# Performance work log

Measured on AMD Instinct MI355X. Metric: run time of the kernel, lower is better.

Reference implementation:

```python
import jax, jax.numpy as jnp
import numpy as np

L, B, D = 2048, 4, 1024
H = 16
DK = D // 2            # q/k dim = 512
GLU_D = 2816
D_CONV = 4
NORMALIZER = 16.0
EPS = 1e-5


def setup_inputs() -> dict:
    key = jax.random.key(0)
    ks = jax.random.split(key, 20)
    s = 0.02
    inp = {
        "x": jax.random.normal(ks[0], (L, B, D), jnp.float32),
        "tn_w": jnp.ones((D,), jnp.float32),
        "tn_b": jnp.zeros((D,), jnp.float32),
        "conv_w": jax.random.normal(ks[1], (D, D_CONV), jnp.float32) * s,  # depthwise kernel (d, w)
        "q_w": jax.random.normal(ks[2], (D, DK), jnp.float32) * s,
        "kg_w": jax.random.normal(ks[3], (D, DK), jnp.float32) * s,
        "v_w": jax.random.normal(ks[4], (D, D), jnp.float32) * s,
        "g_w": jax.random.normal(ks[5], (D, D), jnp.float32) * s,
        "g_b": jnp.zeros((D,), jnp.float32),
        "out_w": jax.random.normal(ks[6], (D, D), jnp.float32) * s,
        "aug_balance": jax.random.normal(ks[7], (DK,), jnp.float32) * s,
        "cn_w": jnp.ones((D,), jnp.float32),
        "cn_b": jnp.zeros((D,), jnp.float32),
        "l1_w": jax.random.normal(ks[8], (D, GLU_D), jnp.float32) * s,
        "l2_w": jax.random.normal(ks[9], (D, GLU_D), jnp.float32) * s,
        "l3_w": jax.random.normal(ks[10], (GLU_D, D), jnp.float32) * s,
    }
    return inp


def _layernorm(y, w, b):
    m = jnp.mean(y, axis=-1, keepdims=True)
    v = jnp.var(y, axis=-1, keepdims=True)
    return (y - m) * jax.lax.rsqrt(v + EPS) * w + b


def _gla_scan(q, k, v, gk):
    # q,k,gk: (B,H,L,dk); v: (B,H,L,dv). Recurrent gated linear attention:
    # S_t = diag(exp(gk_t)) S_{t-1} + k_t v_t^T ; o_t = q_t S_t
    b, h, l, dk = q.shape
    dv = v.shape[-1]
    qT = jnp.moveaxis(q, 2, 0)  # (L,B,H,dk)
    kT = jnp.moveaxis(k, 2, 0)
    vT = jnp.moveaxis(v, 2, 0)
    gT = jnp.moveaxis(gk, 2, 0)

    def step(S, inp):
        q_t, k_t, v_t, g_t = inp
        S = jnp.exp(g_t)[..., None] * S + k_t[..., :, None] * v_t[..., None, :]
        o_t = jnp.einsum('bhk,bhkv->bhv', q_t, S)
        return S, o_t

    S0 = jnp.zeros((b, h, dk, dv), jnp.float32)
    _, o = jax.lax.scan(step, S0, (qT, kT, vT, gT))  # o: (L,B,H,dv)
    return jnp.moveaxis(o, 0, 2)  # (B,H,L,dv)


def reference(x, tn_w, tn_b, conv_w, q_w, kg_w, v_w, g_w, g_b, out_w,
              aug_balance, cn_w, cn_b, l1_w, l2_w, l3_w):
    residual = x  # (L,B,D)
    h = _layernorm(x, tn_w, tn_b)
    h = jnp.transpose(h, (1, 0, 2))  # (B,L,D)

    # causal depthwise conv1d (kernel 4, left pad 3) + SiLU
    hp = jnp.pad(h, ((0, 0), (D_CONV - 1, 0), (0, 0)))
    y = sum(hp[:, i:i + L, :] * conv_w[:, i] for i in range(D_CONV))
    y = jax.nn.silu(y)

    q = y @ q_w                     # (B,L,DK)
    kg = y @ kg_w                   # (B,L,DK)
    v = y @ v_w                     # (B,L,D)
    g = y @ g_w + g_b               # (B,L,D)

    gk = jax.nn.log_sigmoid(kg) / NORMALIZER
    k = 1.0 - jnp.exp(gk)

    dk_h = DK // H   # 32
    dv_h = D // H    # 64
    qh = q.reshape(B, L, H, dk_h).transpose(0, 2, 1, 3).astype(jnp.float32)
    kh = k.reshape(B, L, H, dk_h).transpose(0, 2, 1, 3).astype(jnp.float32)
    vh = v.reshape(B, L, H, dv_h).transpose(0, 2, 1, 3).astype(jnp.float32)
    gh = gk.reshape(B, L, H, dk_h).transpose(0, 2, 1, 3).astype(jnp.float32)
    aug = aug_balance.reshape(H, dk_h).astype(jnp.float32)

    o = _gla_scan(qh, kh, vh, gh)  # (B,H,L,dv_h)

    # self-augmentation term
    aug_w = jnp.einsum('bhld,hd,bhld->bhl', qh, aug, kh)
    o = o + jax.nn.sigmoid(aug_w[..., None] * vh)

    # group norm: LayerNorm over head dim, no affine
    m = jnp.mean(o, axis=-1, keepdims=True)
    var = jnp.var(o, axis=-1, keepdims=True)
    o = (o - m) * jax.lax.rsqrt(var + EPS)
    o = o.transpose(0, 2, 1, 3).reshape(B, L, D).astype(x.dtype)

    o = jax.nn.silu(g) * o
    o = o @ out_w                   # (B,L,D)

    x1 = jnp.transpose(o, (1, 0, 2)) + residual  # back to (L,B,D)

    z = _layernorm(x1, cn_w, cn_b)
    glu = (jax.nn.silu(z @ l1_w) * (z @ l2_w)) @ l3_w
    return glu + x1
```

## Files before the change

kernel.cpp:

```cpp
#include <hip/hip_runtime.h>


#define Lseq 2048
#define Bb 4
#define Dd 1024
#define Hh 16
#define GLUD 2816
#define NC 32
#define CHK 64

typedef float f32x4 __attribute__((ext_vector_type(4)));
typedef __bf16 bf16x8 __attribute__((ext_vector_type(8)));
typedef unsigned short u16;
typedef u16 u16x8 __attribute__((ext_vector_type(8)));

__device__ __forceinline__ u16 f2bf(float f) {
  unsigned int u = __float_as_uint(f);
  u += 0x7fffu + ((u >> 16) & 1u);
  return (u16)(u >> 16);
}

__device__ __forceinline__ int swz(int col, int row) {
  return (col & ~31) | ((((col >> 3) + (row >> 1)) & 3) << 3) | (col & 7);
}

__device__ __forceinline__ void gll16(const void* g, void* l) {
  __builtin_amdgcn_global_load_lds((const __attribute__((address_space(1))) void*)g,
                                   (__attribute__((address_space(3))) void*)l, 16, 0, 0);
}

__device__ __forceinline__ float block_sum(float v, float* red) {
#pragma unroll
  for (int o = 32; o > 0; o >>= 1) v += __shfl_down(v, o);
  __syncthreads();
  if ((threadIdx.x & 63) == 0) red[threadIdx.x >> 6] = v;
  __syncthreads();
  return red[0] + red[1] + red[2] + red[3];
}

__global__ __launch_bounds__(256) void ln1_k(const float* __restrict__ x,
                                             const float* __restrict__ w,
                                             const float* __restrict__ bia,
                                             float* __restrict__ h) {
  __shared__ float red[4];
  int r = blockIdx.x;
  int l = r >> 2, bb = r & 3;
  const float* xr = x + (size_t)r * Dd;
  int d0 = threadIdx.x * 4;
  float4 xv = *(const float4*)&xr[d0];
  float mean = block_sum(xv.x + xv.y + xv.z + xv.w, red) * (1.f / Dd);
  float a0 = xv.x - mean, a1 = xv.y - mean, a2 = xv.z - mean, a3 = xv.w - mean;
  float var = block_sum(a0 * a0 + a1 * a1 + a2 * a2 + a3 * a3, red) * (1.f / Dd);
  float rs = rsqrtf(var + 1e-5f);
  float4 ov;
  ov.x = a0 * rs * w[d0 + 0] + bia[d0 + 0];
  ov.y = a1 * rs * w[d0 + 1] + bia[d0 + 1];
  ov.z = a2 * rs * w[d0 + 2] + bia[d0 + 2];
  ov.w = a3 * rs * w[d0 + 3] + bia[d0 + 3];
  *(float4*)&h[((size_t)(bb * Lseq + l)) * Dd + d0] = ov;
}

__global__ __launch_bounds__(256) void ln2_k(const float* __restrict__ x1,
                                             const float* __restrict__ w,
                                             const float* __restrict__ bia,
                                             u16* __restrict__ z) {
  __shared__ float red[4];
  int r = blockIdx.x;
  const float* xr = x1 + (size_t)r * Dd;
  int d0 = threadIdx.x * 4;
  float4 xv = *(const float4*)&xr[d0];
  float mean = block_sum(xv.x + xv.y + xv.z + xv.w, red) * (1.f / Dd);
  float a0 = xv.x - mean, a1 = xv.y - mean, a2 = xv.z - mean, a3 = xv.w - mean;
  float var = block_sum(a0 * a0 + a1 * a1 + a2 * a2 + a3 * a3, red) * (1.f / Dd);
  float rs = rsqrtf(var + 1e-5f);
  ushort4 o;
  o.x = f2bf(a0 * rs * w[d0 + 0] + bia[d0 + 0]);
  o.y = f2bf(a1 * rs * w[d0 + 1] + bia[d0 + 1]);
  o.z = f2bf(a2 * rs * w[d0 + 2] + bia[d0 + 2]);
  o.w = f2bf(a3 * rs * w[d0 + 3] + bia[d0 + 3]);
  int dcol = (d0 & ~31) | ((((d0 >> 3) + (r >> 1)) & 3) << 3) | (d0 & 7);
  *(ushort4*)&z[(size_t)r * Dd + dcol] = o;
}

__global__ __launch_bounds__(256) void conv_k(const float* __restrict__ h,
                                              const float* __restrict__ cw,
                                              u16* __restrict__ ybf) {
  int m = blockIdx.x;
  int b = m >> 11, l = m & (Lseq - 1);
  int d0 = threadIdx.x * 4;
  float4 acc = {0.f, 0.f, 0.f, 0.f};
  const float* hb = h + ((size_t)b * Lseq) * Dd + d0;
#pragma unroll
  for (int w = 0; w < 4; w++) {
    int ll = l - 3 + w;
    if (ll >= 0) {
      float4 hv = *(const float4*)&hb[(size_t)ll * Dd];
      acc.x += hv.x * cw[(d0 + 0) * 4 + w];
      acc.y += hv.y * cw[(d0 + 1) * 4 + w];
      acc.z += hv.z * cw[(d0 + 2) * 4 + w];
      acc.w += hv.w * cw[(d0 + 3) * 4 + w];
    }
  }
  ushort4 o;
  o.x = f2bf(acc.x / (1.f + expf(-acc.x)));
  o.y = f2bf(acc.y / (1.f + expf(-acc.y)));
  o.z = f2bf(acc.z / (1.f + expf(-acc.z)));
  o.w = f2bf(acc.w / (1.f + expf(-acc.w)));
  int dcol = (d0 & ~31) | ((((d0 >> 3) + (m >> 1)) & 3) << 3) | (d0 & 7);
  *(ushort4*)&ybf[(size_t)m * Dd + dcol] = o;
}

__global__ __launch_bounds__(256) void prep_k(const float* __restrict__ q_w,
                                              const float* __restrict__ kg_w,
                                              const float* __restrict__ v_w,
                                              const float* __restrict__ g_w,
                                              const float* __restrict__ out_w,
                                              const float* __restrict__ l1_w,
                                              const float* __restrict__ l2_w,
                                              const float* __restrict__ l3_w,
                                              u16* __restrict__ Wqkvg,
                                              u16* __restrict__ Wout,
                                              u16* __restrict__ Wl12,
                                              u16* __restrict__ Wl3) {
  __shared__ float tile[32][33];
  int blk = blockIdx.x;
  const float* src;
  u16* dst;
  int R, C, ilv = 0, off = 0, base;
  if (blk < 512)       { src = q_w;   dst = Wqkvg;              R = 1024; C = 512;  base = 0; }
  else if (blk < 1024) { src = kg_w;  dst = Wqkvg + 512 * 1024; R = 1024; C = 512;  base = 512; }
  else if (blk < 2048) { src = v_w;   dst = Wqkvg + 1024 * 1024; R = 1024; C = 1024; base = 1024; }
  else if (blk < 3072) { src = g_w;   dst = Wqkvg + 2048 * 1024; R = 1024; C = 1024; base = 2048; }
  else if (blk < 4096) { src = out_w; dst = Wout;               R = 1024; C = 1024; base = 3072; }
  else if (blk < 6912) { src = l1_w;  dst = Wl12; R = 1024; C = 2816; ilv = 1; off = 0; base = 4096; }
  else if (blk < 9728) { src = l2_w;  dst = Wl12; R = 1024; C = 2816; ilv = 1; off = 1; base = 6912; }
  else                 { src = l3_w;  dst = Wl3;  R = 2816; C = 1024; base = 9728; }
  int local = blk - base;
  int ct = C >> 5;
  int bx = local % ct, by = local / ct;
  int tx = threadIdx.x & 31, ty = threadIdx.x >> 5;
  int c0 = bx * 32, r0 = by * 32;
#pragma unroll
  for (int k = 0; k < 4; k++)
    tile[ty + 8 * k][tx] = src[(size_t)(r0 + ty + 8 * k) * C + c0 + tx];
  __syncthreads();
#pragma unroll
  for (int k = 0; k < 4; k++) {
    int c = c0 + ty + 8 * k;
    int dstrow = ilv ? (((c >> 4) << 5) + off * 16 + (c & 15)) : c;
    int kpos = r0 + tx;
    dst[(size_t)dstrow * R + swz(kpos, dstrow)] = f2bf(tile[tx][ty + 8 * k]);
  }
}

__global__ __launch_bounds__(256) void passA_k(const float* __restrict__ decay,
                                               const float* __restrict__ qkvg,
                                               float* __restrict__ T,
                                               float* __restrict__ P) {
  int wave = threadIdx.x >> 6, lane = threadIdx.x & 63;
  int c = blockIdx.x * 4 + wave, bh = blockIdx.y;
  int b = bh >> 4, h = bh & 15;
  size_t t0 = (size_t)b * Lseq + c * CHK;
  const float* ep = decay + t0 * 512 + h * 32;
  const float* vp = qkvg + t0 * 3072 + 1024 + h * 64 + lane;
  const float* dp = decay + t0 * 512 + h * 32 + (lane & 31);
  float S[32];
#pragma unroll
  for (int i = 0; i < 32; i++) S[i] = 0.f;
  float p = 1.f;
  float vnext = vp[0], dnext = dp[0];
#pragma unroll 1
  for (int ts = 0; ts < CHK; ts++) {
    float vj = vnext, dl = dnext;
    int tn = (ts + 1 < CHK) ? ts + 1 : ts;
    vnext = vp[(size_t)tn * 3072];
    dnext = dp[(size_t)tn * 512];
    const float* e = ep + (size_t)ts * 512;
    p *= dl;
#pragma unroll
    for (int i = 0; i < 32; i++) {
      float ei = e[i];
      float kv = (1.f - ei) * vj;
      S[i] = ei * S[i] + kv;
    }
  }
  float* Tc = T + ((size_t)bh * NC + c) * 2048;
#pragma unroll
  for (int i = 0; i < 32; i++) Tc[i * 64 + lane] = S[i];
  if (lane < 32) P[((size_t)bh * NC + c) * 32 + lane] = p;
}

__global__ __launch_bounds__(256) void passB_k(const float* __restrict__ T,
                                               const float* __restrict__ P,
                                               float* __restrict__ Sg) {
  int bh = blockIdx.x;
  int tid = threadIdx.x;
  int f = tid * 8, i = f >> 6;
  float s[8];
#pragma unroll
  for (int e = 0; e < 8; e++) s[e] = 0.f;
  for (int c = 0; c < NC; c++) {
    size_t base = ((size_t)bh * NC + c) * 2048 + f;
    float pc = P[((size_t)bh * NC + c) * 32 + i];
#pragma unroll
    for (int e = 0; e < 8; e++) {
      float tv = T[base + e];
      Sg[base + e] = s[e];
      s[e] = pc * s[e] + tv;
    }
  }
}

__global__ __launch_bounds__(256) void passC_k(const float* __restrict__ decay,
                                               const float* __restrict__ qkvg,
                                               const float* __restrict__ Sg,
                                               float* __restrict__ osc) {
  int wave = threadIdx.x >> 6, lane = threadIdx.x & 63;
  int c = blockIdx.x * 4 + wave, bh = blockIdx.y;
  int b = bh >> 4, h = bh & 15;
  size_t t0 = (size_t)b * Lseq + c * CHK;
  const float* ep = decay + t0 * 512 + h * 32;
  const float* qp = qkvg + t0 * 3072 + h * 32;
  const float* vp = qkvg + t0 * 3072 + 1024 + h * 64 + lane;
  float* op = osc + t0 * 1024 + h * 64 + lane;
  float S[32];
  const float* Sgc = Sg + ((size_t)bh * NC + c) * 2048;
#pragma unroll
  for (int i = 0; i < 32; i++) S[i] = Sgc[i * 64 + lane];
  float vnext = vp[0];
#pragma unroll 1
  for (int ts = 0; ts < CHK; ts++) {
    float vj = vnext;
    int tn = (ts + 1 < CHK) ? ts + 1 : ts;
    vnext = vp[(size_t)tn * 3072];
    const float* e = ep + (size_t)ts * 512;
    const float* q = qp + (size_t)ts * 3072;
    float a0 = 0.f, a1 = 0.f, a2 = 0.f, a3 = 0.f;
#pragma unroll
    for (int i = 0; i < 32; i += 4) {
      float e0 = e[i], e1 = e[i + 1], e2 = e[i + 2], e3 = e[i + 3];
      S[i + 0] = e0 * S[i + 0] + (1.f - e0) * vj; a0 += q[i + 0] * S[i + 0];
      S[i + 1] = e1 * S[i + 1] + (1.f - e1) * vj; a1 += q[i + 1] * S[i + 1];
      S[i + 2] = e2 * S[i + 2] + (1.f - e2) * vj; a2 += q[i + 2] * S[i + 2];
      S[i + 3] = e3 * S[i + 3] + (1.f - e3) * vj; a3 += q[i + 3] * S[i + 3];
    }
    op[(size_t)ts * 1024] = (a0 + a1) + (a2 + a3);
  }
}

__global__ __launch_bounds__(256) void postscan_k(const float* __restrict__ osc,
                                                  const float* __restrict__ qkvg,
                                                  const float* __restrict__ decay,
                                                  const float* __restrict__ aug,
                                                  const float* __restrict__ gb,
                                                  u16* __restrict__ o2) {
  int m = blockIdx.x;
  int tid = threadIdx.x;
  int h = tid >> 4, t16 = tid & 15;
  int j0 = t16 * 4;
  size_t base = (size_t)m * 3072;
  float4 ov = *(const float4*)&osc[(size_t)m * 1024 + h * 64 + j0];
  int i0 = t16 * 2;
  float q0 = qkvg[base + h * 32 + i0], q1 = qkvg[base + h * 32 + i0 + 1];
  float kA = 1.f - decay[(size_t)m * 512 + h * 32 + i0];
  float kB = 1.f - decay[(size_t)m * 512 + h * 32 + i0 + 1];
  float aw = q0 * aug[h * 32 + i0] * kA + q1 * aug[h * 32 + i0 + 1] * kB;
  aw += __shfl_xor(aw, 1); aw += __shfl_xor(aw, 2);
  aw += __shfl_xor(aw, 4); aw += __shfl_xor(aw, 8);
  float4 vv = *(const float4*)&qkvg[base + 1024 + h * 64 + j0];
  ov.x += 1.f / (1.f + expf(-aw * vv.x));
  ov.y += 1.f / (1.f + expf(-aw * vv.y));
  ov.z += 1.f / (1.f + expf(-aw * vv.z));
  ov.w += 1.f / (1.f + expf(-aw * vv.w));
  float s = ov.x + ov.y + ov.z + ov.w;
  s += __shfl_xor(s, 1); s += __shfl_xor(s, 2);
  s += __shfl_xor(s, 4); s += __shfl_xor(s, 8);
  float mean = s * (1.f / 64.f);
  float d0 = ov.x - mean, d1 = ov.y - mean, d2 = ov.z - mean, d3 = ov.w - mean;
  float ss = d0 * d0 + d1 * d1 + d2 * d2 + d3 * d3;
  ss += __shfl_xor(ss, 1); ss += __shfl_xor(ss, 2);
  ss += __shfl_xor(ss, 4); ss += __shfl_xor(ss, 8);
  float rs = rsqrtf(ss * (1.f / 64.f) + 1e-5f);
  float4 gv = *(const float4*)&qkvg[base + 2048 + h * 64 + j0];
  float g0 = gv.x + gb[h * 64 + j0 + 0];
  float g1 = gv.y + gb[h * 64 + j0 + 1];
  float g2 = gv.z + gb[h * 64 + j0 + 2];
  float g3 = gv.w + gb[h * 64 + j0 + 3];
  ushort4 o;
  o.x = f2bf((g0 / (1.f + expf(-g0))) * d0 * rs);
  o.y = f2bf((g1 / (1.f + expf(-g1))) * d1 * rs);
  o.z = f2bf((g2 / (1.f + expf(-g2))) * d2 * rs);
  o.w = f2bf((g3 / (1.f + expf(-g3))) * d3 * rs);
  int col = h * 64 + j0;
  int dcol = (col & ~31) | ((((col >> 3) + (m >> 1)) & 3) << 3) | (col & 7);
  *(ushort4*)&o2[(size_t)m * 1024 + dcol] = o;
}

template <int EPI>
__global__ __launch_bounds__(256) void gemm_bt(const u16* __restrict__ A,
                                               const u16* __restrict__ B,
                                               int M, int N, int K,
                                               float* __restrict__ Cf,
                                               const float* __restrict__ addsrc,
                                               u16* __restrict__ Cbf,
                                               float* __restrict__ decayp) {
  __shared__ __align__(16) u16 lA[2 * 4096];
  __shared__ __align__(16) u16 lB[2 * 4096];
  const int tid = threadIdx.x;
  const int wave = tid >> 6, lane = tid & 63;
  const int m0 = blockIdx.y * 128, n0 = blockIdx.x * 128;
  const int wm = wave & 1, wn = wave >> 1;
  f32x4 acc[4][4];
#pragma unroll
  for (int a = 0; a < 4; a++)
#pragma unroll
    for (int b = 0; b < 4; b++) acc[a][b] = {0.f, 0.f, 0.f, 0.f};

  const int srow = lane >> 2;
  const int sk8 = (lane & 3) * 8;
  const int rsel = lane & 15;
  const int rot = (((lane >> 4) + (rsel >> 1)) & 3) << 3;
  for (int k0 = 0; k0 < K; k0 += 64) {
    __syncthreads();
#pragma unroll
    for (int g = 0; g < 2; g++) {
#pragma unroll
      for (int it = 0; it < 2; it++) {
        int j = wave * 2 + it;
        int row = j * 16 + srow;
        gll16(A + (size_t)(m0 + row) * K + k0 + g * 32 + sk8, &lA[g * 4096 + j * 512]);
        gll16(B + (size_t)(n0 + row) * K + k0 + g * 32 + sk8, &lB[g * 4096 + j * 512]);
      }
    }
    __syncthreads();
#pragma unroll
    for (int g = 0; g < 2; g++) {
      bf16x8 af[4], bfr[4];
#pragma unroll
      for (int t = 0; t < 4; t++) {
        af[t] = __builtin_bit_cast(bf16x8,
                 *(const u16x8*)&lA[g * 4096 + (wm * 64 + t * 16 + rsel) * 32 + rot]);
        bfr[t] = __builtin_bit_cast(bf16x8,
                 *(const u16x8*)&lB[g * 4096 + (wn * 64 + t * 16 + rsel) * 32 + rot]);
      }
#pragma unroll
      for (int tm = 0; tm < 4; tm++)
#pragma unroll
        for (int tn = 0; tn < 4; tn++)
          acc[tm][tn] = __builtin_amdgcn_mfma_f32_16x16x32_bf16(af[tm], bfr[tn], acc[tm][tn], 0, 0, 0);
    }
  }

  const int rquad = (lane >> 4) * 4;
  const int csel = lane & 15;
#pragma unroll
  for (int tm = 0; tm < 4; tm++) {
    int rowb = m0 + wm * 64 + tm * 16 + rquad;
#pragma unroll
    for (int tn = 0; tn < 4; tn++) {
      int col = n0 + wn * 64 + tn * 16 + csel;
#pragma unroll
      for (int r = 0; r < 4; r++) {
        float v = acc[tm][tn][r];
        int row = rowb + r;
        if (EPI == 0) {
          if (col >= 512 && col < 1024) {
            float sg = 1.f / (1.f + expf(-v));
            decayp[(size_t)row * 512 + (col - 512)] = expf(0.0625f * logf(sg));
          } else {
            Cf[(size_t)row * N + col] = v;
          }
        } else if (EPI == 1) {
          int l = row & (Lseq - 1), bb = row >> 11;
          size_t o = ((size_t)(l * Bb + bb)) * Dd + col;
          Cf[o] = v + addsrc[o];
        } else if (EPI == 2) {
          size_t o = (size_t)row * Dd + col;
          Cf[o] = v + addsrc[o];
        } else {
          if ((tn & 1) == 0) {
            float u2 = acc[tm][tn + 1][r];
            float p = (v / (1.f + expf(-v))) * u2;
            int oc = (n0 >> 1) + wn * 32 + ((tn >> 1) << 4) + csel;
            Cbf[(size_t)row * (N >> 1) + swz(oc, row)] = f2bf(p);
          }
        }
      }
    }
  }
}

extern "C" void kernel_launch(void* const* d_in, const int* in_sizes, int n_in,
                              void* d_out, int out_size, void* d_ws, size_t ws_size,
                              hipStream_t stream) {
  const float* x = (const float*)d_in[0];
  const float* tn_w = (const float*)d_in[1];
  const float* tn_b = (const float*)d_in[2];
  const float* conv_w = (const float*)d_in[3];
  const float* q_w = (const float*)d_in[4];
  const float* kg_w = (const float*)d_in[5];
  const float* v_w = (const float*)d_in[6];
  const float* g_w = (const float*)d_in[7];
  const float* g_b = (const float*)d_in[8];
  const float* out_w = (const float*)d_in[9];
  const float* aug = (const float*)d_in[10];
  const float* cn_w = (const float*)d_in[11];
  const float* cn_b = (const float*)d_in[12];
  const float* l1_w = (const float*)d_in[13];
  const float* l2_w = (const float*)d_in[14];
  const float* l3_w = (const float*)d_in[15];
  float* out = (float*)d_out;
  char* ws = (char*)d_ws;

  u16* Wqkvg = (u16*)(ws + 0);
  u16* Wout = (u16*)(ws + 6291456);
  u16* Wl12 = (u16*)(ws + 8388608);
  u16* Wl3 = (u16*)(ws + 19922944);
  float* hbuf = (float*)(ws + 25690112);
  float* osc = hbuf;
  u16* ybf = (u16*)(ws + 59244544);
  u16* o2bf = (u16*)(ws + 59244544);
  float* qkvg = (float*)(ws + 76021760);
  float* x1 = (float*)(ws + 76021760);
  u16* zbf = (u16*)(ws + 109576192);
  u16* pbf = (u16*)(ws + 126353408);
  float* decay = (float*)(ws + 176685056);
  float* Tbuf = (float*)(ws + 193462272);
  float* Sg = Tbuf;
  float* Pbuf = (float*)(ws + 210239488);

  dim3 b256(256);
  prep_k<<<12544, b256, 0, stream>>>(q_w, kg_w, v_w, g_w, out_w, l1_w, l2_w, l3_w,
                                     Wqkvg, Wout, Wl12, Wl3);
  ln1_k<<<8192, b256, 0, stream>>>(x, tn_w, tn_b, hbuf);
  conv_k<<<8192, b256, 0, stream>>>(hbuf, conv_w, ybf);
  gemm_bt<0><<<dim3(24, 64), b256, 0, stream>>>(ybf, Wqkvg, 8192, 3072, 1024, qkvg, nullptr, nullptr, decay);
  passA_k<<<dim3(NC / 4, 64), b256, 0, stream>>>(decay, qkvg, Tbuf, Pbuf);
  passB_k<<<64, b256, 0, stream>>>(Tbuf, Pbuf, Sg);
  passC_k<<<dim3(NC / 4, 64), b256, 0, stream>>>(decay, qkvg, Sg, osc);
  postscan_k<<<8192, b256, 0, stream>>>(osc, qkvg, decay, aug, g_b, o2bf);
  gemm_bt<1><<<dim3(8, 64), b256, 0, stream>>>(o2bf, Wout, 8192, 1024, 1024, x1, x, nullptr, nullptr);
  ln2_k<<<8192, b256, 0, stream>>>(x1, cn_w, cn_b, zbf);
  gemm_bt<3><<<dim3(44, 64), b256, 0, stream>>>(zbf, Wl12, 8192, 5632, 1024, nullptr, nullptr, pbf, nullptr);
  gemm_bt<2><<<dim3(8, 64), b256, 0, stream>>>(pbf, Wl3, 8192, 1024, 2816, out, x1, nullptr, nullptr);
}
```

Before: 709.7 us.

## Store q/v/g projections as bf16 and fuse post-scan epilogue into passC

The QKVG GEMM epilogue now writes q, v and g as bf16 instead of fp32, halving the traffic the scan kernels read. The postscan kernel is folded into passC, which now computes the self-augmentation sigmoid, the per-head group norm via 64-lane shuffles, and the silu gating, then writes swizzled bf16 output directly. This removes the fp32 osc round trip and one launch. The cost is a lower-precision q/v/g path and more per-timestep work (two full-wave reductions and exps) inside the sequential scan loop.

New measurement: 697.7 us. About the same (-1.7%).

```diff
diff --git a/kernel.cpp b/kernel.cpp
--- a/kernel.cpp
+++ b/kernel.cpp
@@ -18,6 +18,9 @@
   unsigned int u = __float_as_uint(f);
   u += 0x7fffu + ((u >> 16) & 1u);
   return (u16)(u >> 16);
+}
+__device__ __forceinline__ float bf2f(u16 b) {
+  return __uint_as_float(((unsigned int)b) << 16);
 }
 
 __device__ __forceinline__ int swz(int col, int row) {
@@ -154,7 +157,7 @@
 }
 
 __global__ __launch_bounds__(256) void passA_k(const float* __restrict__ decay,
-                                               const float* __restrict__ qkvg,
+                                               const u16* __restrict__ qkvg16,
                                                float* __restrict__ T,
                                                float* __restrict__ P) {
   int wave = threadIdx.x >> 6, lane = threadIdx.x & 63;
@@ -162,16 +165,17 @@
   int b = bh >> 4, h = bh & 15;
   size_t t0 = (size_t)b * Lseq + c * CHK;
   const float* ep = decay + t0 * 512 + h * 32;
-  const float* vp = qkvg + t0 * 3072 + 1024 + h * 64 + lane;
+  const u16* vp = qkvg16 + t0 * 3072 + 1024 + h * 64 + lane;
   const float* dp = decay + t0 * 512 + h * 32 + (lane & 31);
   float S[32];
 #pragma unroll
   for (int i = 0; i < 32; i++) S[i] = 0.f;
   float p = 1.f;
-  float vnext = vp[0], dnext = dp[0];
+  u16 vnext = vp[0];
+  float dnext = dp[0];
 #pragma unroll 1
   for (int ts = 0; ts < CHK; ts++) {
-    float vj = vnext, dl = dnext;
+    float vj = bf2f(vnext), dl = dnext;
     int tn = (ts + 1 < CHK) ? ts + 1 : ts;
     vnext = vp[(size_t)tn * 3072];
     dnext = dp[(size_t)tn * 512];
@@ -212,88 +216,66 @@
 }
 
 __global__ __launch_bounds__(256) void passC_k(const float* __restrict__ decay,
-                                               const float* __restrict__ qkvg,
+                                               const u16* __restrict__ qkvg16,
                                                const float* __restrict__ Sg,
-                                               float* __restrict__ osc) {
+                                               const float* __restrict__ aug,
+                                               const float* __restrict__ gb,
+                                               u16* __restrict__ o2) {
   int wave = threadIdx.x >> 6, lane = threadIdx.x & 63;
   int c = blockIdx.x * 4 + wave, bh = blockIdx.y;
   int b = bh >> 4, h = bh & 15;
   size_t t0 = (size_t)b * Lseq + c * CHK;
   const float* ep = decay + t0 * 512 + h * 32;
-  const float* qp = qkvg + t0 * 3072 + h * 32;
-  const float* vp = qkvg + t0 * 3072 + 1024 + h * 64 + lane;
-  float* op = osc + t0 * 1024 + h * 64 + lane;
+  const unsigned int* qp = (const unsigned int*)(qkvg16 + t0 * 3072 + h * 32);
+  const u16* vp = qkvg16 + t0 * 3072 + 1024 + h * 64 + lane;
+  const u16* gp = qkvg16 + t0 * 3072 + 2048 + h * 64 + lane;
   float S[32];
   const float* Sgc = Sg + ((size_t)bh * NC + c) * 2048;
 #pragma unroll
   for (int i = 0; i < 32; i++) S[i] = Sgc[i * 64 + lane];
-  float vnext = vp[0];
+  float vaug[32];
+#pragma unroll
+  for (int i = 0; i < 32; i++) vaug[i] = aug[h * 32 + i];
+  float gbv = gb[h * 64 + lane];
+  int colbase = h * 64 + lane;
+  int colfix = (colbase & ~31) | (colbase & 7);
+  int colrot0 = colbase >> 3;
+  u16 vnext = vp[0], gnext = gp[0];
 #pragma unroll 1
   for (int ts = 0; ts < CHK; ts++) {
-    float vj = vnext;
+    float vj = bf2f(vnext);
+    float gg = bf2f(gnext) + gbv;
     int tn = (ts + 1 < CHK) ? ts + 1 : ts;
     vnext = vp[(size_t)tn * 3072];
+    gnext = gp[(size_t)tn * 3072];
     const float* e = ep + (size_t)ts * 512;
-    const float* q = qp + (size_t)ts * 3072;
-    float a0 = 0.f, a1 = 0.f, a2 = 0.f, a3 = 0.f;
-#pragma unroll
-    for (int i = 0; i < 32; i += 4) {
-      float e0 = e[i], e1 = e[i + 1], e2 = e[i + 2], e3 = e[i + 3];
-      S[i + 0] = e0 * S[i + 0] + (1.f - e0) * vj; a0 += q[i + 0] * S[i + 0];
-      S[i + 1] = e1 * S[i + 1] + (1.f - e1) * vj; a1 += q[i + 1] * S[i + 1];
-      S[i + 2] = e2 * S[i + 2] + (1.f - e2) * vj; a2 += q[i + 2] * S[i + 2];
-      S[i + 3] = e3 * S[i + 3] + (1.f - e3) * vj; a3 += q[i + 3] * S[i + 3];
-    }
-    op[(size_t)ts * 1024] = (a0 + a1) + (a2 + a3);
-  }
-}
-
-__global__ __launch_bounds__(256) void postscan_k(const float* __restrict__ osc,
-                                                  const float* __restrict__ qkvg,
-                                                  const float* __restrict__ decay,
-                                                  const float* __restrict__ aug,
-                                                  const float* __restrict__ gb,
-                                                  u16* __restrict__ o2) {
-  int m = blockIdx.x;
-  int tid = threadIdx.x;
-  int h = tid >> 4, t16 = tid & 15;
-  int j0 = t16 * 4;
-  size_t base = (size_t)m * 3072;
-  float4 ov = *(const float4*)&osc[(size_t)m * 1024 + h * 64 + j0];
-  int i0 = t16 * 2;
-  float q0 = qkvg[base + h * 32 + i0], q1 = qkvg[base + h * 32 + i0 + 1];
-  float kA = 1.f - decay[(size_t)m * 512 + h * 32 + i0];
-  float kB = 1.f - decay[(size_t)m * 512 + h * 32 + i0 + 1];
-  float aw = q0 * aug[h * 32 + i0] * kA + q1 * aug[h * 32 + i0 + 1] * kB;
-  aw += __shfl_xor(aw, 1); aw += __shfl_xor(aw, 2);
-  aw += __shfl_xor(aw, 4); aw += __shfl_xor(aw, 8);
-  float4 vv = *(const float4*)&qkvg[base + 1024 + h * 64 + j0];
-  ov.x += 1.f / (1.f + expf(-aw * vv.x));
-  ov.y += 1.f / (1.f + expf(-aw * vv.y));
-  ov.z += 1.f / (1.f + expf(-aw * vv.z));
-  ov.w += 1.f / (1.f + expf(-aw * vv.w));
-  float s = ov.x + ov.y + ov.z + ov.w;
-  s += __shfl_xor(s, 1); s += __shfl_xor(s, 2);
-  s += __shfl_xor(s, 4); s += __shfl_xor(s, 8);
-  float mean = s * (1.f / 64.f);
-  float d0 = ov.x - mean, d1 = ov.y - mean, d2 = ov.z - mean, d3 = ov.w - mean;
-  float ss = d0 * d0 + d1 * d1 + d2 * d2 + d3 * d3;
-  ss += __shfl_xor(ss, 1); ss += __shfl_xor(ss, 2);
-  ss += __shfl_xor(ss, 4); ss += __shfl_xor(ss, 8);
-  float rs = rsqrtf(ss * (1.f / 64.f) + 1e-5f);
-  float4 gv = *(const float4*)&qkvg[base + 2048 + h * 64 + j0];
-  float g0 = gv.x + gb[h * 64 + j0 + 0];
-  float g1 = gv.y + gb[h * 64 + j0 + 1];
-  float g2 = gv.z + gb[h * 64 + j0 + 2];
-  float g3 = gv.w + gb[h * 64 + j0 + 3];
-  ushort4 o;
-  o.x = f2bf((g0 / (1.f + expf(-g0))) * d0 * rs);
-  o.y = f2bf((g1 / (1.f + expf(-g1))) * d1 * rs);
-  o.z = f2bf((g2 / (1.f + expf(-g2))) * d2 * rs);
-  o.w = f2bf((g3 / (1.f + expf(-g3))) * d3 * rs);
-  int col = h * 64 + j0;
-  int dcol = (col & ~31) | ((((col >> 3) + (m >> 1)) & 3) << 3) | (col & 7);
-  *(ushort4*)&o2[(size_t)m * 1024 + dcol] = o;
+    const unsigned int* q = qp + (size_t)ts * 1536;
+    float a0 = 0.f, a1 = 0.f, aw = 0.f;
+#pragma unroll
+    for (int i = 0; i < 32; i += 2) {
+      unsigned int qq = q[i >> 1];
+      float q0 = __uint_as_float(qq << 16);
+      float q1 = __uint_as_float(qq & 0xffff0000u);
+      float e0 = e[i], e1 = e[i + 1];
+      float k0 = 1.f - e0, k1 = 1.f - e1;
+      S[i + 0] = e0 * S[i + 0] + k0 * vj; a0 += q0 * S[i + 0];
+      S[i + 1] = e1 * S[i + 1] + k1 * vj; a1 += q1 * S[i + 1];
+      aw += q0 * vaug[i] * k0 + q1 * vaug[i + 1] * k1;
+    }
+    float o = (a0 + a1) + 1.f / (1.f + expf(-aw * vj));
+    float s = o;
+#pragma unroll
+    for (int d = 1; d < 64; d <<= 1) s += __shfl_xor(s, d);
+    float dcen = o - s * (1.f / 64.f);
+    float ss = dcen * dcen;
+#pragma unroll
+    for (int d = 1; d < 64; d <<= 1) ss += __shfl_xor(ss, d);
+    float rs = rsqrtf(ss * (1.f / 64.f) + 1e-5f);
+    float res = (gg / (1.f + expf(-gg))) * dcen * rs;
+    int m = (int)t0 + ts;
+    int dcol = colfix | (((colrot0 + (m >> 1)) & 3) << 3);
+    o2[(size_t)m * 1024 + dcol] = f2bf(res);
+  }
 }
 
 template <int EPI>
@@ -368,7 +350,7 @@
             float sg = 1.f / (1.f + expf(-v));
             decayp[(size_t)row * 512 + (col - 512)] = expf(0.0625f * logf(sg));
           } else {
-            Cf[(size_t)row * N + col] = v;
+            Cbf[(size_t)row * N + col] = f2bf(v);
           }
         } else if (EPI == 1) {
           int l = row & (Lseq - 1), bb = row >> 11;
@@ -417,28 +399,26 @@
   u16* Wl12 = (u16*)(ws + 8388608);
   u16* Wl3 = (u16*)(ws + 19922944);
   float* hbuf = (float*)(ws + 25690112);
-  float* osc = hbuf;
+  float* x1 = hbuf;
   u16* ybf = (u16*)(ws + 59244544);
   u16* o2bf = (u16*)(ws + 59244544);
-  float* qkvg = (float*)(ws + 76021760);
-  float* x1 = (float*)(ws + 76021760);
-  u16* zbf = (u16*)(ws + 109576192);
+  u16* qkvg16 = (u16*)(ws + 76021760);
+  u16* zbf = (u16*)(ws + 76021760);
   u16* pbf = (u16*)(ws + 126353408);
-  float* decay = (float*)(ws + 176685056);
-  float* Tbuf = (float*)(ws + 193462272);
+  float* decay = (float*)(ws + 172490752);
+  float* Tbuf = (float*)(ws + 189267968);
   float* Sg = Tbuf;
-  float* Pbuf = (float*)(ws + 210239488);
+  float* Pbuf = (float*)(ws + 206045184);
 
   dim3 b256(256);
   prep_k<<<12544, b256, 0, stream>>>(q_w, kg_w, v_w, g_w, out_w, l1_w, l2_w, l3_w,
                                      Wqkvg, Wout, Wl12, Wl3);
   ln1_k<<<8192, b256, 0, stream>>>(x, tn_w, tn_b, hbuf);
   conv_k<<<8192, b256, 0, stream>>>(hbuf, conv_w, ybf);
-  gemm_bt<0><<<dim3(24, 64), b256, 0, stream>>>(ybf, Wqkvg, 8192, 3072, 1024, qkvg, nullptr, nullptr, decay);
-  passA_k<<<dim3(NC / 4, 64), b256, 0, stream>>>(decay, qkvg, Tbuf, Pbuf);
+  gemm_bt<0><<<dim3(24, 64), b256, 0, stream>>>(ybf, Wqkvg, 8192, 3072, 1024, nullptr, nullptr, qkvg16, decay);
+  passA_k<<<dim3(NC / 4, 64), b256, 0, stream>>>(decay, qkvg16, Tbuf, Pbuf);
   passB_k<<<64, b256, 0, stream>>>(Tbuf, Pbuf, Sg);
-  passC_k<<<dim3(NC / 4, 64), b256, 0, stream>>>(decay, qkvg, Sg, osc);
-  postscan_k<<<8192, b256, 0, stream>>>(osc, qkvg, decay, aug, g_b, o2bf);
+  passC_k<<<dim3(NC / 4, 64), b256, 0, stream>>>(decay, qkvg16, Sg, aug, g_b, o2bf);
   gemm_bt<1><<<dim3(8, 64), b256, 0, stream>>>(o2bf, Wout, 8192, 1024, 1024, x1, x, nullptr, nullptr);
   ln2_k<<<8192, b256, 0, stream>>>(x1, cn_w, cn_b, zbf);
   gemm_bt<3><<<dim3(44, 64), b256, 0, stream>>>(zbf, Wl12, 8192, 5632, 1024, nullptr, nullptr, pbf, nullptr);
```
